# Performance work log

Measured on AMD Instinct MI355X. Metric: run time of the kernel, lower is better.

The kernel has to match this reference:

```python
import jax, jax.numpy as jnp
import numpy as np

EPS = 1e-8
COS_SCALE = 20.0
COS_POWER = 1
NEG_MODE = 3
NUM_CLASSES = 60
INPUT_SIZE = 2048
REG_FC_CH = 2048
BOX_DIM = 4
N = 16384


def _l2n(v, axis=-1):
    # matches F.cosine_similarity: divide by max(||v||, eps) per vector
    n = jnp.sqrt(jnp.sum(v * v, axis=axis, keepdims=True))
    return v / jnp.maximum(n, EPS)


def setup_inputs() -> dict:
    key = jax.random.key(0)
    ks = jax.random.split(key, 8)
    x = jax.random.normal(ks[0], (N, INPUT_SIZE), dtype=jnp.float32)
    # reps: nn.Linear(input_size, num_classes+1), std=0.01 init
    reps_w = 0.01 * jax.random.normal(ks[1], (NUM_CLASSES + 1, INPUT_SIZE), dtype=jnp.float32)
    # neg_reps: nn.Linear(input_size, num_classes*neg_mode, bias=False), std=0.01
    neg_reps_w = 0.01 * jax.random.normal(ks[2], (NUM_CLASSES * NEG_MODE, INPUT_SIZE), dtype=jnp.float32)
    # reg_fc: Linear(input_size, reg_fc_channels), std=0.01, bias 0
    reg_fc_w = 0.01 * jax.random.normal(ks[3], (REG_FC_CH, INPUT_SIZE), dtype=jnp.float32)
    reg_fc_b = jnp.zeros((REG_FC_CH,), dtype=jnp.float32)
    # bbox_pred: Linear(reg_fc_channels, num_classes*box_dim), std=0.001, bias 0
    bbox_w = 0.001 * jax.random.normal(ks[4], (NUM_CLASSES * BOX_DIM, REG_FC_CH), dtype=jnp.float32)
    bbox_b = jnp.zeros((NUM_CLASSES * BOX_DIM,), dtype=jnp.float32)
    return {"x": x, "reps_w": reps_w, "neg_reps_w": neg_reps_w,
            "reg_fc_w": reg_fc_w, "reg_fc_b": reg_fc_b,
            "bbox_w": bbox_w, "bbox_b": bbox_b}


def reference(x, reps_w, neg_reps_w, reg_fc_w, reg_fc_b, bbox_w, bbox_b):
    h = x @ reg_fc_w.T + reg_fc_b                      # [N, reg_fc_ch]
    proposal_deltas = h @ bbox_w.T + bbox_b            # [N, num_classes*box_dim]

    # cosine similarity vs class prototypes (drop last background row)
    reps = reps_w[:-1, :]                              # [C, D]
    xn = _l2n(x)                                       # [N, D]
    rn = _l2n(reps)                                    # [C, D]
    cos_sim = xn @ rn.T                                # [N, C]

    # negative prototypes: [C, M, D], cosine then max over M
    neg_reps = neg_reps_w.reshape(NUM_CLASSES, NEG_MODE, INPUT_SIZE)
    nrn = _l2n(neg_reps)                               # [C, M, D]
    neg_all = jnp.einsum('nd,cmd->ncm', xn, nrn)       # [N, C, M]
    neg_cos_sim = jnp.max(neg_all, axis=2)             # [N, C]

    neg_scores = jnp.exp(-((1.0 - neg_cos_sim) ** COS_POWER) * COS_SCALE)
    scores_ori = jnp.exp(-((1.0 - cos_sim) ** COS_POWER) * COS_SCALE)

    bg_pad = jnp.full((scores_ori.shape[0], 1), -100000.0, dtype=scores_ori.dtype)
    scores = jnp.concatenate([scores_ori, bg_pad], axis=1)  # [N, C+1]
    return (scores, proposal_deltas, cos_sim, neg_cos_sim, neg_scores)
```

## Files before the change

kernel.cpp:

```cpp
#include <hip/hip_runtime.h>
#include <stdint.h>

#define KD 2048
#define NROWS 16384

typedef float f32x4 __attribute__((ext_vector_type(4)));
typedef __bf16 bf16x8 __attribute__((ext_vector_type(8)));
typedef unsigned short u16x8 __attribute__((ext_vector_type(8)));
typedef unsigned short u16x4 __attribute__((ext_vector_type(4)));

#define OFF_DELTAS 999424
#define OFF_COS    4931584
#define OFF_NEGC   5914624
#define OFF_NEGS   6897664

__device__ inline unsigned short f2bf(float f) {
  union { float f; unsigned u; } v; v.f = f;
  unsigned u = v.u;
  return (unsigned short)((u + 0x7FFFu + ((u >> 16) & 1u)) >> 16);
}

__device__ inline void gload_lds16(const void* g, void* l) {
  __builtin_amdgcn_global_load_lds(
      (const __attribute__((address_space(1))) void*)g,
      (__attribute__((address_space(3))) void*)l,
      16, 0, 0);
}

__global__ __launch_bounds__(512, 2)
void gemm256(const unsigned short* __restrict__ A,
             const unsigned short* __restrict__ B,
             float* __restrict__ Sf,
             float* __restrict__ Df,
             const float* __restrict__ invn,
             const float* __restrict__ bfold,
             int nNtiles)
{
  __shared__ __align__(16) char lds[3 * 49152];
  const int bid = blockIdx.x;
  const int bm = bid / nNtiles, bn = bid % nNtiles;
  const size_t row0 = (size_t)bm * 256, col0 = (size_t)bn * 128;
  const int tid = threadIdx.x, lane = tid & 63, wv = tid >> 6;
  const int wm = wv >> 1, wn = wv & 1;
  const int fr = lane & 15, fq = lane >> 4;
  const char* Ab = (const char*)(A + row0 * KD);
  const char* Bb = (const char*)(B + col0 * KD);
  f32x4 acc[4][4] = {};

  int aoff[4], aG[4], boff[2], bG[2];
#pragma unroll
  for (int s = 0; s < 4; ++s) {
    const int o = (tid + s * 512) * 16;
    const int r = o >> 7;
    aoff[s] = o;
    aG[s] = r * (KD * 2) + ((o & 127) ^ ((r & 7) << 4));
  }
#pragma unroll
  for (int s = 0; s < 2; ++s) {
    const int o = (tid + s * 512) * 16;
    const int r = o >> 7;
    boff[s] = o;
    bG[s] = r * (KD * 2) + ((o & 127) ^ ((r & 7) << 4));
  }

  auto stage = [&](int kt, int b) {
    char* bufA = lds + b * 49152;
    char* bufB = bufA + 32768;
    const int kby = kt * 128;
#pragma unroll
    for (int s = 0; s < 4; ++s)
      gload_lds16(Ab + (size_t)(aG[s] + kby), bufA + aoff[s]);
#pragma unroll
    for (int s = 0; s < 2; ++s)
      gload_lds16(Bb + (size_t)(bG[s] + kby), bufB + boff[s]);
  };

  const int sw = (fr & 7) << 4;

  auto compute = [&](int b) {
    const char* bufA = lds + b * 49152;
    const char* bufB = bufA + 32768;
    bf16x8 af[4][2], bfv[4][2];
#pragma unroll
    for (int m = 0; m < 4; ++m) {
      const char* base = bufA + (wm * 64 + m * 16 + fr) * 128;
#pragma unroll
      for (int kk = 0; kk < 2; ++kk)
        af[m][kk] = *(const bf16x8*)(base + ((kk * 64 + fq * 16) ^ sw));
    }
#pragma unroll
    for (int n = 0; n < 4; ++n) {
      const char* base = bufB + (wn * 64 + n * 16 + fr) * 128;
#pragma unroll
      for (int kk = 0; kk < 2; ++kk)
        bfv[n][kk] = *(const bf16x8*)(base + ((kk * 64 + fq * 16) ^ sw));
    }
    __builtin_amdgcn_s_setprio(1);
#pragma unroll
    for (int m = 0; m < 4; ++m)
#pragma unroll
      for (int n = 0; n < 4; ++n)
#pragma unroll
        for (int kk = 0; kk < 2; ++kk)
          acc[m][n] = __builtin_amdgcn_mfma_f32_16x16x32_bf16(af[m][kk], bfv[n][kk], acc[m][n], 0, 0, 0);
    __builtin_amdgcn_s_setprio(0);
  };

  const int NT = KD / 64;
  stage(0, 0);
  stage(1, 1);
  asm volatile("s_waitcnt vmcnt(6)" ::: "memory");
  __builtin_amdgcn_sched_barrier(0);
  __builtin_amdgcn_s_barrier();
  __builtin_amdgcn_sched_barrier(0);

  int cur = 0;
#pragma unroll 1
  for (int t = 0; t < NT; ++t) {
    if (t + 2 < NT) {
      int nb = cur + 2; if (nb >= 3) nb -= 3;
      stage(t + 2, nb);
    }
    compute(cur);
    if (t + 1 < NT) {
      if (t + 2 < NT) asm volatile("s_waitcnt vmcnt(6)" ::: "memory");
      else            asm volatile("s_waitcnt vmcnt(0)" ::: "memory");
      __builtin_amdgcn_sched_barrier(0);
      __builtin_amdgcn_s_barrier();
      __builtin_amdgcn_sched_barrier(0);
    }
    if (++cur == 3) cur = 0;
  }

#pragma unroll
  for (int m = 0; m < 4; ++m) {
    const size_t rb = row0 + wm * 64 + m * 16 + fq * 4;
#pragma unroll
    for (int n = 0; n < 4; ++n) {
      const int c = (int)col0 + wn * 64 + n * 16 + fr;
      if (bn < 2) {
#pragma unroll
        for (int j = 0; j < 4; ++j) {
          const size_t r = rb + j;
          Sf[r * 256 + c] = acc[m][n][j] * invn[r];
        }
      } else {
        const int c2 = c - 256;
        if (c2 < 240) {
          const float bv = bfold[c2];
#pragma unroll
          for (int j = 0; j < 4; ++j)
            Df[(rb + j) * 240 + c2] = acc[m][n][j] + bv;
        }
      }
    }
  }
}

template<int EPI>
__global__ __launch_bounds__(256)
void gemm_bt(const unsigned short* __restrict__ A,
             const unsigned short* __restrict__ B,
             unsigned short* __restrict__ Cb,
             int nNtiles, int ldc)
{
  __shared__ unsigned short sA[128 * 64];
  __shared__ unsigned short sB[128 * 64];
  const int bid = blockIdx.x;
  const int bm = bid / nNtiles, bn = bid % nNtiles;
  const size_t row0 = (size_t)bm * 128, col0 = (size_t)bn * 128;
  const int tid = threadIdx.x, lane = tid & 63, wv = tid >> 6;
  const char* Ab = (const char*)(A + row0 * KD);
  const char* Bb = (const char*)(B + col0 * KD);
  const int wr = (wv >> 1) * 64, wc = (wv & 1) * 64;
  const int fr = lane & 15, fq = lane >> 4;
  f32x4 acc[4][4] = {};
  const int so = wv * 1024 + lane * 16;

  for (int kt = 0; kt < KD / 64; ++kt) {
    const int kbyte = kt * 128;
#pragma unroll
    for (int i = 0; i < 4; ++i) {
      const int o = i * 4096 + so;
      const int r = o >> 7, cb = o & 127;
      gload_lds16(Ab + (size_t)r * (KD * 2) + kbyte + cb, (char*)sA + o);
      gload_lds16(Bb + (size_t)r * (KD * 2) + kbyte + cb, (char*)sB + o);
    }
    __syncthreads();
#pragma unroll
    for (int kk = 0; kk < 2; ++kk) {
      bf16x8 af[4], bfr[4];
#pragma unroll
      for (int m = 0; m < 4; ++m)
        af[m] = *(const bf16x8*)((const char*)sA + (wr + m * 16 + fr) * 128 + kk * 64 + fq * 16);
#pragma unroll
      for (int n = 0; n < 4; ++n)
        bfr[n] = *(const bf16x8*)((const char*)sB + (wc + n * 16 + fr) * 128 + kk * 64 + fq * 16);
#pragma unroll
      for (int m = 0; m < 4; ++m)
#pragma unroll
        for (int n = 0; n < 4; ++n)
          acc[m][n] = __builtin_amdgcn_mfma_f32_16x16x32_bf16(af[m], bfr[n], acc[m][n], 0, 0, 0);
    }
    __syncthreads();
  }

#pragma unroll
  for (int m = 0; m < 4; ++m) {
    const size_t rb = row0 + wr + m * 16 + fq * 4;
#pragma unroll
    for (int n = 0; n < 4; ++n) {
      const int c = (int)col0 + wc + n * 16 + fr;
#pragma unroll
      for (int j = 0; j < 4; ++j)
        Cb[(rb + j) * (size_t)ldc + c] = f2bf(acc[m][n][j]);
    }
  }
}

__global__ __launch_bounds__(256)
void prep_x(const float* __restrict__ x, unsigned short* __restrict__ xbf,
            float* __restrict__ invn)
{
  const int n = blockIdx.x, tid = threadIdx.x;
  const float4* row = (const float4*)(x + (size_t)n * KD);
  float4 a = row[tid * 2], b = row[tid * 2 + 1];
  float ss = a.x * a.x + a.y * a.y + a.z * a.z + a.w * a.w
           + b.x * b.x + b.y * b.y + b.z * b.z + b.w * b.w;
#pragma unroll
  for (int off = 32; off > 0; off >>= 1) ss += __shfl_down(ss, off);
  __shared__ float red[4];
  if ((tid & 63) == 0) red[tid >> 6] = ss;
  __syncthreads();
  if (tid == 0) {
    const float tot = red[0] + red[1] + red[2] + red[3];
    invn[n] = 1.f / fmaxf(sqrtf(tot), 1e-8f);
  }
  u16x8 o;
  o[0] = f2bf(a.x); o[1] = f2bf(a.y); o[2] = f2bf(a.z); o[3] = f2bf(a.w);
  o[4] = f2bf(b.x); o[5] = f2bf(b.y); o[6] = f2bf(b.z); o[7] = f2bf(b.w);
  *(u16x8*)(xbf + (size_t)n * KD + (size_t)tid * 8) = o;
}

__global__ __launch_bounds__(256)
void trans_w1(const float* __restrict__ w1, unsigned short* __restrict__ w1t)
{
  __shared__ float t[64][65];
  const int i0 = (blockIdx.x & 31) * 64;
  const int j0 = (blockIdx.x >> 5) * 64;
  const int tid = threadIdx.x;
  const int r = tid >> 4, c4 = tid & 15;
#pragma unroll
  for (int rr = 0; rr < 4; ++rr) {
    const int row = r + rr * 16;
    const float4 v = *(const float4*)(w1 + (size_t)(i0 + row) * KD + j0 + c4 * 4);
    t[row][c4 * 4 + 0] = v.x; t[row][c4 * 4 + 1] = v.y;
    t[row][c4 * 4 + 2] = v.z; t[row][c4 * 4 + 3] = v.w;
  }
  __syncthreads();
#pragma unroll
  for (int rr = 0; rr < 4; ++rr) {
    const int jrow = r + rr * 16;
    u16x4 o;
    o[0] = f2bf(t[c4 * 4 + 0][jrow]); o[1] = f2bf(t[c4 * 4 + 1][jrow]);
    o[2] = f2bf(t[c4 * 4 + 2][jrow]); o[3] = f2bf(t[c4 * 4 + 3][jrow]);
    *(u16x4*)(w1t + (size_t)(j0 + jrow) * KD + i0 + c4 * 4) = o;
  }
}

__global__ __launch_bounds__(256)
void bfold_k(const float* __restrict__ w2, const float* __restrict__ b1,
             const float* __restrict__ b2, float* __restrict__ bf)
{
  const int c = blockIdx.x, tid = threadIdx.x;
  const float4* row = (const float4*)(w2 + (size_t)c * KD);
  const float4* bb  = (const float4*)b1;
  float4 a = row[tid * 2], b = row[tid * 2 + 1];
  float4 p = bb[tid * 2],  q = bb[tid * 2 + 1];
  float ss = a.x * p.x + a.y * p.y + a.z * p.z + a.w * p.w
           + b.x * q.x + b.y * q.y + b.z * q.z + b.w * q.w;
#pragma unroll
  for (int off = 32; off > 0; off >>= 1) ss += __shfl_down(ss, off);
  __shared__ float red[4];
  if ((tid & 63) == 0) red[tid >> 6] = ss;
  __syncthreads();
  if (tid == 0) bf[c] = red[0] + red[1] + red[2] + red[3] + b2[c];
}

__global__ __launch_bounds__(256)
void prep_rows(const float* __restrict__ reps, const float* __restrict__ negrep,
               const float* __restrict__ bbox,
               unsigned short* __restrict__ Big, unsigned short* __restrict__ W2)
{
  const int r = blockIdx.x, tid = threadIdx.x;
  const u16x8 z = {0, 0, 0, 0, 0, 0, 0, 0};
  if (r < 256) {
    unsigned short* dst = Big + (size_t)r * KD;
    if (r >= 240) { *(u16x8*)(dst + (size_t)tid * 8) = z; return; }
    const float* src = (r < 60) ? reps + (size_t)r * KD
                                : negrep + (size_t)(r - 60) * KD;
    const float4* p = (const float4*)src;
    float4 a = p[tid * 2], b = p[tid * 2 + 1];
    float ss = a.x * a.x + a.y * a.y + a.z * a.z + a.w * a.w
             + b.x * b.x + b.y * b.y + b.z * b.z + b.w * b.w;
#pragma unroll
    for (int off = 32; off > 0; off >>= 1) ss += __shfl_down(ss, off);
    __shared__ float red[4];
    if ((tid & 63) == 0) red[tid >> 6] = ss;
    __syncthreads();
    const float iv = 1.f / fmaxf(sqrtf(red[0] + red[1] + red[2] + red[3]), 1e-8f);
    u16x8 o;
    o[0] = f2bf(a.x * iv); o[1] = f2bf(a.y * iv); o[2] = f2bf(a.z * iv); o[3] = f2bf(a.w * iv);
    o[4] = f2bf(b.x * iv); o[5] = f2bf(b.y * iv); o[6] = f2bf(b.z * iv); o[7] = f2bf(b.w * iv);
    *(u16x8*)(dst + (size_t)tid * 8) = o;
  } else {
    const int rr = r - 256;
    unsigned short* dst = W2 + (size_t)rr * KD;
    if (rr >= 240) { *(u16x8*)(dst + (size_t)tid * 8) = z; return; }
    const float4* p = (const float4*)(bbox + (size_t)rr * KD);
    float4 a = p[tid * 2], b = p[tid * 2 + 1];
    u16x8 o;
    o[0] = f2bf(a.x); o[1] = f2bf(a.y); o[2] = f2bf(a.z); o[3] = f2bf(a.w);
    o[4] = f2bf(b.x); o[5] = f2bf(b.y); o[6] = f2bf(b.z); o[7] = f2bf(b.w);
    *(u16x8*)(dst + (size_t)tid * 8) = o;
  }
}

__global__ __launch_bounds__(64)
void post(const float* __restrict__ S, float* __restrict__ out)
{
  const int n = blockIdx.x, c = threadIdx.x;
  const float* s = S + (size_t)n * 256;
  float* scores = out;
  float* cosv   = out + OFF_COS;
  float* negc   = out + OFF_NEGC;
  float* negs   = out + OFF_NEGS;
  if (c < 60) {
    const float cs = s[c];
    cosv[(size_t)n * 60 + c]   = cs;
    scores[(size_t)n * 61 + c] = expf(-(1.f - cs) * 20.f);
    const float m3 = fmaxf(s[60 + 3 * c], fmaxf(s[61 + 3 * c], s[62 + 3 * c]));
    negc[(size_t)n * 60 + c] = m3;
    negs[(size_t)n * 60 + c] = expf(-(1.f - m3) * 20.f);
  } else if (c == 60) {
    scores[(size_t)n * 61 + 60] = -100000.0f;
  }
}

extern "C" void kernel_launch(void* const* d_in, const int* in_sizes, int n_in,
                              void* d_out, int out_size, void* d_ws, size_t ws_size,
                              hipStream_t stream)
{
  const float* x      = (const float*)d_in[0];
  const float* reps   = (const float*)d_in[1];
  const float* negrep = (const float*)d_in[2];
  const float* w1     = (const float*)d_in[3];
  const float* b1     = (const float*)d_in[4];
  const float* w2     = (const float*)d_in[5];
  const float* b2     = (const float*)d_in[6];
  float* out = (float*)d_out;

  char* w = (char*)d_ws;
  float*          S    = (float*)(w);
  unsigned short* Big  = (unsigned short*)(w + 16777216);
  unsigned short* W1T  = (unsigned short*)(w + 18874368);
  unsigned short* W2bf = (unsigned short*)(w + 27262976);
  float*          invn = (float*)(w + 28311552);
  float*          bfold= (float*)(w + 28377088);
  unsigned short* xbf  = (unsigned short*)(w + 28378112);

  prep_x   <<<NROWS, 256, 0, stream>>>(x, xbf, invn);
  trans_w1 <<<1024, 256, 0, stream>>>(w1, W1T);
  prep_rows<<<512, 256, 0, stream>>>(reps, negrep, w2, Big, W2bf);
  bfold_k  <<<240, 256, 0, stream>>>(w2, b1, b2, bfold);

  gemm_bt<3><<<2 * 16, 256, 0, stream>>>(W2bf, W1T, Big + 256 * (size_t)KD, 16, 2048);

  gemm256<<<64 * 4, 512, 0, stream>>>(xbf, Big, S, out + OFF_DELTAS, invn, bfold, 4);

  post<<<NROWS, 64, 0, stream>>>(S, out);
}
```

Baseline: 322.0 us.

## Fuse cosine post-processing into main GEMM epilogue and split-K the weight fold

The main GEMM is retiled to 128x256 blocks so one column tile holds all 256 similarity columns. Its epilogue normalizes them through LDS and writes scores, cos, neg-cos and neg-scores directly, which removes the separate post kernel and the S scratch round trip. The small W2·W1 fold GEMM, which launched only 32 blocks, is split along K into 8 chunks (256 blocks) that write fp32 partials, followed by a reduce-and-convert kernel. This trades extra partial-sum memory traffic and a slower strided epilogue for better occupancy in the fold and fewer launches.

```diff
diff --git a/kernel.cpp b/kernel.cpp
--- a/kernel.cpp
+++ b/kernel.cpp
@@ -30,33 +30,31 @@
 __global__ __launch_bounds__(512, 2)
 void gemm256(const unsigned short* __restrict__ A,
              const unsigned short* __restrict__ B,
-             float* __restrict__ Sf,
-             float* __restrict__ Df,
+             float* __restrict__ out,
              const float* __restrict__ invn,
-             const float* __restrict__ bfold,
-             int nNtiles)
+             const float* __restrict__ bfold)
 {
   __shared__ __align__(16) char lds[3 * 49152];
   const int bid = blockIdx.x;
-  const int bm = bid / nNtiles, bn = bid % nNtiles;
-  const size_t row0 = (size_t)bm * 256, col0 = (size_t)bn * 128;
+  const int bm = bid >> 1, bn = bid & 1;
+  const size_t row0 = (size_t)bm * 128, col0 = (size_t)bn * 256;
   const int tid = threadIdx.x, lane = tid & 63, wv = tid >> 6;
-  const int wm = wv >> 1, wn = wv & 1;
+  const int wm = wv >> 2, wn = wv & 3;
   const int fr = lane & 15, fq = lane >> 4;
   const char* Ab = (const char*)(A + row0 * KD);
   const char* Bb = (const char*)(B + col0 * KD);
   f32x4 acc[4][4] = {};
 
-  int aoff[4], aG[4], boff[2], bG[2];
-#pragma unroll
-  for (int s = 0; s < 4; ++s) {
+  int aoff[2], aG[2], boff[4], bG[4];
+#pragma unroll
+  for (int s = 0; s < 2; ++s) {
     const int o = (tid + s * 512) * 16;
     const int r = o >> 7;
     aoff[s] = o;
     aG[s] = r * (KD * 2) + ((o & 127) ^ ((r & 7) << 4));
   }
 #pragma unroll
-  for (int s = 0; s < 2; ++s) {
+  for (int s = 0; s < 4; ++s) {
     const int o = (tid + s * 512) * 16;
     const int r = o >> 7;
     boff[s] = o;
@@ -65,13 +63,13 @@
 
   auto stage = [&](int kt, int b) {
     char* bufA = lds + b * 49152;
-    char* bufB = bufA + 32768;
+    char* bufB = bufA + 16384;
     const int kby = kt * 128;
 #pragma unroll
+    for (int s = 0; s < 2; ++s)
+      gload_lds16(Ab + (size_t)(aG[s] + kby), bufA + aoff[s]);
+#pragma unroll
     for (int s = 0; s < 4; ++s)
-      gload_lds16(Ab + (size_t)(aG[s] + kby), bufA + aoff[s]);
-#pragma unroll
-    for (int s = 0; s < 2; ++s)
       gload_lds16(Bb + (size_t)(bG[s] + kby), bufB + boff[s]);
   };
 
@@ -79,7 +77,7 @@
 
   auto compute = [&](int b) {
     const char* bufA = lds + b * 49152;
-    const char* bufB = bufA + 32768;
+    const char* bufB = bufA + 16384;
     bf16x8 af[4][2], bfv[4][2];
 #pragma unroll
     for (int m = 0; m < 4; ++m) {
@@ -132,42 +130,66 @@
     if (++cur == 3) cur = 0;
   }
 
-#pragma unroll
-  for (int m = 0; m < 4; ++m) {
-    const size_t rb = row0 + wm * 64 + m * 16 + fq * 4;
+  __syncthreads();
+  if (bn == 1) {
+    float* Df = out + OFF_DELTAS;
 #pragma unroll
     for (int n = 0; n < 4; ++n) {
-      const int c = (int)col0 + wn * 64 + n * 16 + fr;
-      if (bn < 2) {
-#pragma unroll
-        for (int j = 0; j < 4; ++j) {
-          const size_t r = rb + j;
-          Sf[r * 256 + c] = acc[m][n][j] * invn[r];
-        }
-      } else {
-        const int c2 = c - 256;
-        if (c2 < 240) {
-          const float bv = bfold[c2];
+      const int c = wn * 64 + n * 16 + fr;
+      if (c < 240) {
+        const float bv = bfold[c];
+#pragma unroll
+        for (int m = 0; m < 4; ++m) {
+          const size_t rb = row0 + wm * 64 + m * 16 + fq * 4;
 #pragma unroll
           for (int j = 0; j < 4; ++j)
-            Df[(rb + j) * 240 + c2] = acc[m][n][j] + bv;
+            Df[(rb + j) * 240 + c] = acc[m][n][j] + bv;
         }
       }
     }
-  }
-}
-
-template<int EPI>
-__global__ __launch_bounds__(256)
-void gemm_bt(const unsigned short* __restrict__ A,
-             const unsigned short* __restrict__ B,
-             unsigned short* __restrict__ Cb,
-             int nNtiles, int ldc)
+  } else {
+    float* sT = (float*)lds;
+#pragma unroll
+    for (int m = 0; m < 4; ++m) {
+      const int rl = wm * 64 + m * 16 + fq * 4;
+#pragma unroll
+      for (int j = 0; j < 4; ++j) {
+        const float iv = invn[row0 + rl + j];
+#pragma unroll
+        for (int n = 0; n < 4; ++n)
+          sT[(rl + j) * 256 + wn * 64 + n * 16 + fr] = acc[m][n][j] * iv;
+      }
+    }
+    __syncthreads();
+    float* scores = out + row0 * 61;
+    float* cosv   = out + OFF_COS  + row0 * 60;
+    float* negc   = out + OFF_NEGC + row0 * 60;
+    float* negs   = out + OFF_NEGS + row0 * 60;
+    for (int i = tid; i < 128 * 61; i += 512) {
+      const int r = i / 61, c = i - r * 61;
+      scores[i] = (c == 60) ? -100000.0f : expf(-(1.f - sT[r * 256 + c]) * 20.f);
+    }
+    for (int i = tid; i < 128 * 60; i += 512) {
+      const int r = i / 60, c = i - r * 60;
+      const float* sr = sT + r * 256;
+      cosv[i] = sr[c];
+      const float m3 = fmaxf(sr[60 + 3 * c], fmaxf(sr[61 + 3 * c], sr[62 + 3 * c]));
+      negc[i] = m3;
+      negs[i] = expf(-(1.f - m3) * 20.f);
+    }
+  }
+}
+
+__global__ __launch_bounds__(256)
+void fold_split(const unsigned short* __restrict__ A,
+                const unsigned short* __restrict__ B,
+                float* __restrict__ Wpart)
 {
   __shared__ unsigned short sA[128 * 64];
   __shared__ unsigned short sB[128 * 64];
   const int bid = blockIdx.x;
-  const int bm = bid / nNtiles, bn = bid % nNtiles;
+  const int chunk = bid >> 5, rem = bid & 31;
+  const int bm = rem >> 4, bn = rem & 15;
   const size_t row0 = (size_t)bm * 128, col0 = (size_t)bn * 128;
   const int tid = threadIdx.x, lane = tid & 63, wv = tid >> 6;
   const char* Ab = (const char*)(A + row0 * KD);
@@ -177,7 +199,7 @@
   f32x4 acc[4][4] = {};
   const int so = wv * 1024 + lane * 16;
 
-  for (int kt = 0; kt < KD / 64; ++kt) {
+  for (int kt = chunk * 4; kt < chunk * 4 + 4; ++kt) {
     const int kbyte = kt * 128;
 #pragma unroll
     for (int i = 0; i < 4; ++i) {
@@ -205,6 +227,7 @@
     __syncthreads();
   }
 
+  float* Wp = Wpart + (size_t)chunk * 240 * KD;
 #pragma unroll
   for (int m = 0; m < 4; ++m) {
     const size_t rb = row0 + wr + m * 16 + fq * 4;
@@ -212,10 +235,33 @@
     for (int n = 0; n < 4; ++n) {
       const int c = (int)col0 + wc + n * 16 + fr;
 #pragma unroll
-      for (int j = 0; j < 4; ++j)
-        Cb[(rb + j) * (size_t)ldc + c] = f2bf(acc[m][n][j]);
-    }
-  }
+      for (int j = 0; j < 4; ++j) {
+        const size_t r = rb + j;
+        if (r < 240) Wp[r * KD + c] = acc[m][n][j];
+      }
+    }
+  }
+}
+
+__global__ __launch_bounds__(256)
+void cvt_fold(const float* __restrict__ Wpart, unsigned short* __restrict__ BigHi)
+{
+  const int b = blockIdx.x, tid = threadIdx.x;
+  unsigned short* dst = BigHi + (size_t)b * KD + (size_t)tid * 8;
+  if (b >= 240) { *(u16x8*)dst = (u16x8){0,0,0,0,0,0,0,0}; return; }
+  const size_t base = (size_t)b * KD + (size_t)tid * 8;
+  float s[8] = {};
+#pragma unroll
+  for (int ch = 0; ch < 8; ++ch) {
+    const float4* p = (const float4*)(Wpart + (size_t)ch * 240 * KD + base);
+    float4 a = p[0], q = p[1];
+    s[0] += a.x; s[1] += a.y; s[2] += a.z; s[3] += a.w;
+    s[4] += q.x; s[5] += q.y; s[6] += q.z; s[7] += q.w;
+  }
+  u16x8 o;
+#pragma unroll
+  for (int e = 0; e < 8; ++e) o[e] = f2bf(s[e]);
+  *(u16x8*)dst = o;
 }
 
 __global__ __launch_bounds__(256)
@@ -326,27 +372,6 @@
   }
 }
 
-__global__ __launch_bounds__(64)
-void post(const float* __restrict__ S, float* __restrict__ out)
-{
-  const int n = blockIdx.x, c = threadIdx.x;
-  const float* s = S + (size_t)n * 256;
-  float* scores = out;
-  float* cosv   = out + OFF_COS;
-  float* negc   = out + OFF_NEGC;
-  float* negs   = out + OFF_NEGS;
-  if (c < 60) {
-    const float cs = s[c];
-    cosv[(size_t)n * 60 + c]   = cs;
-    scores[(size_t)n * 61 + c] = expf(-(1.f - cs) * 20.f);
-    const float m3 = fmaxf(s[60 + 3 * c], fmaxf(s[61 + 3 * c], s[62 + 3 * c]));
-    negc[(size_t)n * 60 + c] = m3;
-    negs[(size_t)n * 60 + c] = expf(-(1.f - m3) * 20.f);
-  } else if (c == 60) {
-    scores[(size_t)n * 61 + 60] = -100000.0f;
-  }
-}
-
 extern "C" void kernel_launch(void* const* d_in, const int* in_sizes, int n_in,
                               void* d_out, int out_size, void* d_ws, size_t ws_size,
                               hipStream_t stream)
@@ -361,22 +386,21 @@
   float* out = (float*)d_out;
 
   char* w = (char*)d_ws;
-  float*          S    = (float*)(w);
-  unsigned short* Big  = (unsigned short*)(w + 16777216);
-  unsigned short* W1T  = (unsigned short*)(w + 18874368);
-  unsigned short* W2bf = (unsigned short*)(w + 27262976);
-  float*          invn = (float*)(w + 28311552);
-  float*          bfold= (float*)(w + 28377088);
-  unsigned short* xbf  = (unsigned short*)(w + 28378112);
+  unsigned short* Big  = (unsigned short*)(w);
+  unsigned short* W1T  = (unsigned short*)(w + 2097152);
+  unsigned short* W2bf = (unsigned short*)(w + 10485760);
+  float*          invn = (float*)(w + 11534336);
+  float*          bfold= (float*)(w + 11599872);
+  float*          Wpart= (float*)(w + 11603968);
+  unsigned short* xbf  = (unsigned short*)(w + 27332608);
 
   prep_x   <<<NROWS, 256, 0, stream>>>(x, xbf, invn);
   trans_w1 <<<1024, 256, 0, stream>>>(w1, W1T);
   prep_rows<<<512, 256, 0, stream>>>(reps, negrep, w2, Big, W2bf);
   bfold_k  <<<240, 256, 0, stream>>>(w2, b1, b2, bfold);
 
-  gemm_bt<3><<<2 * 16, 256, 0, stream>>>(W2bf, W1T, Big + 256 * (size_t)KD, 16, 2048);
-
-  gemm256<<<64 * 4, 512, 0, stream>>>(xbf, Big, S, out + OFF_DELTAS, invn, bfold, 4);
-
-  post<<<NROWS, 64, 0, stream>>>(S, out);
-}
+  fold_split<<<256, 256, 0, stream>>>(W2bf, W1T, Wpart);
+  cvt_fold  <<<256, 256, 0, stream>>>(Wpart, Big + 256 * (size_t)KD);
+
+  gemm256<<<128 * 2, 512, 0, stream>>>(xbf, Big, out, invn, bfold);
+}
```

Result: faster. 285.2 us (-11.4%).
